# Performance work log

Hardware: AMD Instinct MI355X
Metric: run time of the kernel (lower is better)

## Reference

```python
import jax, jax.numpy as jnp
import numpy as np

B, S, D, H = 2, 2048, 1024, 16
HD = D // H  # head_dim = 64

def setup_inputs() -> dict:
    key = jax.random.key(0)
    ks = jax.random.split(key, 11)
    s = 1.0 / np.sqrt(D)
    return {
        "query_input": jax.random.normal(ks[0], (B, S, D), jnp.float32),
        "key_input":   jax.random.normal(ks[1], (B, S, D), jnp.float32),
        "value_input": jax.random.normal(ks[2], (B, S, D), jnp.float32),
        "Wq": jax.random.normal(ks[3], (D, D), jnp.float32) * s,
        "bq": jnp.zeros((D,), jnp.float32),
        "Wk": jax.random.normal(ks[4], (D, D), jnp.float32) * s,
        "bk": jnp.zeros((D,), jnp.float32),
        "Wv": jax.random.normal(ks[5], (D, D), jnp.float32) * s,
        "bv": jnp.zeros((D,), jnp.float32),
        "Wo": jax.random.normal(ks[6], (D, D), jnp.float32) * s,
        "bo": jnp.zeros((D,), jnp.float32),
    }

def _split_heads(x):
    b, s, _ = x.shape
    return x.reshape(b, s, H, HD).transpose(0, 2, 1, 3)  # [B,H,S,HD]

def reference(query_input, key_input, value_input, Wq, bq, Wk, bk, Wv, bv, Wo, bo):
    q = _split_heads(query_input @ Wq + bq)
    k = _split_heads(key_input @ Wk + bk)
    v = _split_heads(value_input @ Wv + bv)
    scores = jnp.einsum('bhqd,bhkd->bhqk', q, k) / jnp.sqrt(jnp.float32(HD))
    attn = jax.nn.softmax(scores, axis=-1)
    out = jnp.einsum('bhqk,bhkd->bhqd', attn, v)
    out = out.transpose(0, 2, 1, 3).reshape(query_input.shape[0], -1, H * HD)
    return out @ Wo + bo
```

## Files before the change

### kernel.cpp

```cpp
#include <hip/hip_runtime.h>
#include <hip/hip_bf16.h>
#include <math.h>

#define B_  2
#define S_  2048
#define D_  1024
#define H_  16
#define HD_ 64

typedef __bf16  bf16x8   __attribute__((ext_vector_type(8)));
typedef float   floatx4  __attribute__((ext_vector_type(4)));
typedef float   floatx16 __attribute__((ext_vector_type(16)));

#define MFMA16(a, b, c) __builtin_amdgcn_mfma_f32_16x16x32_bf16((a), (b), (c), 0, 0, 0)
#define MFMA32(a, b, c) __builtin_amdgcn_mfma_f32_32x32x16_bf16((a), (b), (c), 0, 0, 0)

__device__ __forceinline__ void load_lds16(const void* g, void* l) {
    __builtin_amdgcn_global_load_lds(
        (const __attribute__((address_space(1))) unsigned int*)g,
        (__attribute__((address_space(3))) unsigned int*)l, 16, 0, 0);
}

__device__ __forceinline__ unsigned pk_bf16(float a, float b) {
    unsigned r;
    asm("v_cvt_pk_bf16_f32 %0, %1, %2" : "=v"(r) : "v"(a), "v"(b));
    return r;
}

__device__ __forceinline__ float exp2_hw(float x) {
    float r;
    asm("v_exp_f32 %0, %1" : "=v"(r) : "v"(x));
    return r;
}

__global__ __launch_bounds__(256) void cast3_bf16_k(
    const float* __restrict__ x0, const float* __restrict__ x1, const float* __restrict__ x2,
    __hip_bfloat16* __restrict__ o0, __hip_bfloat16* __restrict__ o1, __hip_bfloat16* __restrict__ o2)
{
    const int z = blockIdx.y;
    const float* src = (z == 0) ? x0 : (z == 1) ? x1 : x2;
    __hip_bfloat16* dst = (z == 0) ? o0 : (z == 1) ? o1 : o2;
    const int i = blockIdx.x * 256 + threadIdx.x;
    const float4* s4 = (const float4*)src;
    const float4 a = s4[2 * i + 0];
    const float4 b = s4[2 * i + 1];
    union { __hip_bfloat16 h[8]; uint4 v; } p;
    p.h[0] = __float2bfloat16(a.x); p.h[1] = __float2bfloat16(a.y);
    p.h[2] = __float2bfloat16(a.z); p.h[3] = __float2bfloat16(a.w);
    p.h[4] = __float2bfloat16(b.x); p.h[5] = __float2bfloat16(b.y);
    p.h[6] = __float2bfloat16(b.z); p.h[7] = __float2bfloat16(b.w);
    ((uint4*)dst)[i] = p.v;
}

__global__ __launch_bounds__(256) void transpose4_cast_k(
    const float* __restrict__ W0, const float* __restrict__ W1,
    const float* __restrict__ W2, const float* __restrict__ W3,
    __hip_bfloat16* __restrict__ T0, __hip_bfloat16* __restrict__ T1,
    __hip_bfloat16* __restrict__ T2, __hip_bfloat16* __restrict__ T3)
{
    const int z = blockIdx.z;
    const float* W = (z == 0) ? W0 : (z == 1) ? W1 : (z == 2) ? W2 : W3;
    __hip_bfloat16* Wt = (z == 0) ? T0 : (z == 1) ? T1 : (z == 2) ? T2 : T3;

    __shared__ float T[64][65];
    const int t  = threadIdx.x;
    const int n0 = blockIdx.x * 64, k0 = blockIdx.y * 64;
    #pragma unroll
    for (int i = 0; i < 4; ++i) {
        const int u = t + i * 256;
        const int r = u >> 4, c4 = (u & 15) * 4;
        const float4 v = *(const float4*)(W + (size_t)(k0 + r) * D_ + n0 + c4);
        T[r][c4 + 0] = v.x; T[r][c4 + 1] = v.y; T[r][c4 + 2] = v.z; T[r][c4 + 3] = v.w;
    }
    __syncthreads();
    #pragma unroll
    for (int i = 0; i < 4; ++i) {
        const int u = t + i * 256;
        const int n = u >> 4, c4 = (u & 15) * 4;
        union { __hip_bfloat16 h[4]; uint2 v; } p;
        #pragma unroll
        for (int j = 0; j < 4; ++j) p.h[j] = __float2bfloat16(T[c4 + j][n]);
        *(uint2*)(Wt + (size_t)(n0 + n) * D_ + k0 + c4) = p.v;
    }
}

__global__ __launch_bounds__(256) void gemm_qkv_k(
    const __hip_bfloat16* __restrict__ xq, const __hip_bfloat16* __restrict__ xk,
    const __hip_bfloat16* __restrict__ xv,
    const __hip_bfloat16* __restrict__ WqT, const __hip_bfloat16* __restrict__ WkT,
    const __hip_bfloat16* __restrict__ WvT,
    const float* __restrict__ bq, const float* __restrict__ bk, const float* __restrict__ bv,
    __hip_bfloat16* __restrict__ Qh, __hip_bfloat16* __restrict__ Kh,
    __hip_bfloat16* __restrict__ Vt)
{
    constexpr int K = 1024;
    __shared__ __align__(16) short As0[128][32], As1[128][32];
    __shared__ __align__(16) short Bs0[128][32], Bs1[128][32];

    const int z = blockIdx.z;
    const __hip_bfloat16* A  = (z == 0) ? xq  : (z == 1) ? xk  : xv;
    const __hip_bfloat16* Bt = (z == 0) ? WqT : (z == 1) ? WkT : WvT;
    const float* bias        = (z == 0) ? bq  : (z == 1) ? bk  : bv;

    const int t    = threadIdx.x;
    const int lane = t & 63, w = t >> 6;
    const int quad = lane >> 4, l16 = lane & 15;
    const int m0   = blockIdx.x * 128, n0 = blockIdx.y * 128;
    const int wm   = (w >> 1) * 64,    wn = (w & 1) * 64;

    floatx4 acc[4][4] = {};

    auto stage = [&](int k0, short (*As)[32], short (*Bs)[32]) {
        #pragma unroll
        for (int i = 0; i < 2; ++i) {
            const int c = t + i * 256;
            const int m = c >> 2, kq = (c ^ (m >> 1)) & 3;
            load_lds16(A + (size_t)(m0 + m) * K + k0 + kq * 8, &As[0][0] + c * 8);
        }
        #pragma unroll
        for (int i = 0; i < 2; ++i) {
            const int c = t + i * 256;
            const int n = c >> 2, kq = (c ^ (n >> 1)) & 3;
            load_lds16(Bt + (size_t)(n0 + n) * K + k0 + kq * 8, &Bs[0][0] + c * 8);
        }
    };

    auto compute = [&](short (*As)[32], short (*Bs)[32]) {
        bf16x8 af[4], bfr[4];
        #pragma unroll
        for (int mt = 0; mt < 4; ++mt) {
            const int r = wm + mt * 16 + l16;
            af[mt]  = *(const bf16x8*)&As[r][((quad ^ (r >> 1)) & 3) * 8];
        }
        #pragma unroll
        for (int nt = 0; nt < 4; ++nt) {
            const int n = wn + nt * 16 + l16;
            bfr[nt] = *(const bf16x8*)&Bs[n][((quad ^ (n >> 1)) & 3) * 8];
        }
        #pragma unroll
        for (int mt = 0; mt < 4; ++mt)
            #pragma unroll
            for (int nt = 0; nt < 4; ++nt)
                acc[mt][nt] = MFMA16(af[mt], bfr[nt], acc[mt][nt]);
    };

    stage(0, As0, Bs0);
    for (int k0 = 0; k0 < K; k0 += 64) {
        __syncthreads();
        stage(k0 + 32, As1, Bs1);
        compute(As0, Bs0);
        __syncthreads();
        if (k0 + 64 < K) stage(k0 + 64, As0, Bs0);
        compute(As1, Bs1);
    }

    if (z != 2) {
        const float oscale = (z == 0) ? 0.125f * 1.44269504088896f : 1.0f;
        __hip_bfloat16* outp = (z == 0) ? Qh : Kh;
        #pragma unroll
        for (int mt = 0; mt < 4; ++mt)
            #pragma unroll
            for (int nt = 0; nt < 4; ++nt) {
                const int gn = n0 + wn + nt * 16 + l16;
                const float bi = bias[gn];
                #pragma unroll
                for (int r = 0; r < 4; ++r) {
                    const int gm = m0 + wm + mt * 16 + quad * 4 + r;
                    const float v = (acc[mt][nt][r] + bi) * oscale;
                    outp[(((size_t)(gm >> 11) * H_ + (gn >> 6)) * S_ + (gm & 2047)) * 64 + (gn & 63)] =
                        __float2bfloat16(v);
                }
            }
    } else {
        #pragma unroll
        for (int mt = 0; mt < 4; ++mt)
            #pragma unroll
            for (int nt = 0; nt < 4; ++nt) {
                const int gn = n0 + wn + nt * 16 + l16;
                const float bi = bias[gn];
                const int gm0 = m0 + wm + mt * 16 + quad * 4;
                union { __hip_bfloat16 h[4]; uint2 u; } pk;
                #pragma unroll
                for (int r = 0; r < 4; ++r) pk.h[r] = __float2bfloat16(acc[mt][nt][r] + bi);
                *(uint2*)(Vt + (((size_t)(gm0 >> 11) * H_ + (gn >> 6)) * 64 + (gn & 63)) * S_ +
                          (gm0 & 2047)) = pk.u;
            }
    }
}

__global__ __launch_bounds__(256) void gemm_oproj_k(
    const __hip_bfloat16* __restrict__ A, const __hip_bfloat16* __restrict__ Bt,
    const float* __restrict__ bias, float* __restrict__ out)
{
    constexpr int K = 1024, N = 1024;
    __shared__ __align__(16) short As0[128][32], As1[128][32];
    __shared__ __align__(16) short Bs0[64][32],  Bs1[64][32];

    const int t    = threadIdx.x;
    const int lane = t & 63, w = t >> 6;
    const int quad = lane >> 4, l16 = lane & 15;
    const int m0   = blockIdx.x * 128, n0 = blockIdx.y * 64;
    const int wm   = (w >> 1) * 64,    wn = (w & 1) * 32;

    floatx4 acc[4][2] = {};

    auto stage = [&](int k0, short (*As)[32], short (*Bs)[32]) {
        #pragma unroll
        for (int i = 0; i < 2; ++i) {
            const int c = t + i * 256;
            const int m = c >> 2, kq = (c ^ (m >> 1)) & 3;
            load_lds16(A + (size_t)(m0 + m) * K + k0 + kq * 8, &As[0][0] + c * 8);
        }
        {
            const int c = t;
            const int n = c >> 2, kq = (c ^ (n >> 1)) & 3;
            load_lds16(Bt + (size_t)(n0 + n) * K + k0 + kq * 8, &Bs[0][0] + c * 8);
        }
    };

    auto compute = [&](short (*As)[32], short (*Bs)[32]) {
        bf16x8 af[4], bfr[2];
        #pragma unroll
        for (int mt = 0; mt < 4; ++mt) {
            const int r = wm + mt * 16 + l16;
            af[mt]  = *(const bf16x8*)&As[r][((quad ^ (r >> 1)) & 3) * 8];
        }
        #pragma unroll
        for (int nt = 0; nt < 2; ++nt) {
            const int n = wn + nt * 16 + l16;
            bfr[nt] = *(const bf16x8*)&Bs[n][((quad ^ (n >> 1)) & 3) * 8];
        }
        #pragma unroll
        for (int mt = 0; mt < 4; ++mt)
            #pragma unroll
            for (int nt = 0; nt < 2; ++nt)
                acc[mt][nt] = MFMA16(af[mt], bfr[nt], acc[mt][nt]);
    };

    stage(0, As0, Bs0);
    for (int k0 = 0; k0 < K; k0 += 64) {
        __syncthreads();
        stage(k0 + 32, As1, Bs1);
        compute(As0, Bs0);
        __syncthreads();
        if (k0 + 64 < K) stage(k0 + 64, As0, Bs0);
        compute(As1, Bs1);
    }

    #pragma unroll
    for (int mt = 0; mt < 4; ++mt)
        #pragma unroll
        for (int nt = 0; nt < 2; ++nt) {
            const int gn = n0 + wn + nt * 16 + l16;
            const float bi = bias[gn];
            #pragma unroll
            for (int r = 0; r < 4; ++r) {
                const int gm = m0 + wm + mt * 16 + quad * 4 + r;
                out[(size_t)gm * N + gn] = acc[mt][nt][r] + bi;
            }
        }
}

union AttnSmem {
    struct { short K0[2][64][64], K1[2][64][64], V0[2][64][64], V1[2][64][64]; } s;
    struct { float O[4][64][33]; float L[4][32]; } c;
};

__global__ __launch_bounds__(512) void attn_mfma_k(
    const __hip_bfloat16* __restrict__ Qh, const __hip_bfloat16* __restrict__ Kh,
    const __hip_bfloat16* __restrict__ Vt, __hip_bfloat16* __restrict__ Ctx)
{
    __shared__ __align__(16) AttnSmem sm;

    const int t    = threadIdx.x;
    const int lane = t & 63, w = t >> 6;
    const int l32  = lane & 31, hi = lane >> 5;
    const int wq   = w & 3, half = w >> 2;
    const int ht   = t & 255;
    const int b = blockIdx.z, h = blockIdx.x;
    const size_t bh = (size_t)b * H_ + h;
    const int q0 = blockIdx.y * 128;
    const int kvbase = half * 16;

    bf16x8 qf[4];
    {
        const __hip_bfloat16* qb = Qh + (bh * S_ + q0 + wq * 32 + l32) * 64 + hi * 8;
        #pragma unroll
        for (int ks = 0; ks < 4; ++ks) qf[ks] = *(const bf16x8*)(qb + ks * 16);
    }

    floatx16 oacc[2] = {};
    float ls = 0.f;

    auto stage = [&](int kt, short (*Ks)[64], short (*Vs)[64]) {
        #pragma unroll
        for (int i = 0; i < 2; ++i) {
            const int c = ht + i * 256;
            const int p = c >> 3, kq = (c ^ p) & 7;
            load_lds16(Kh + (bh * S_ + kt * 64 + p) * 64 + kq * 8, &Ks[0][0] + c * 8);
            load_lds16(Vt + (bh * 64 + p) * S_ + kt * 64 + kq * 8, &Vs[0][0] + c * 8);
        }
    };

    auto mkfrags = [&](const float (&e)[16], bf16x8* fr) {
        #pragma unroll
        for (int k2 = 0; k2 < 2; ++k2) {
            unsigned y0 = pk_bf16(e[8 * k2 + 0], e[8 * k2 + 1]);
            unsigned y1 = pk_bf16(e[8 * k2 + 2], e[8 * k2 + 3]);
            unsigned y2 = pk_bf16(e[8 * k2 + 4], e[8 * k2 + 5]);
            unsigned y3 = pk_bf16(e[8 * k2 + 6], e[8 * k2 + 7]);
            asm volatile("v_permlane32_swap_b32 %0, %1" : "+v"(y0), "+v"(y2));
            asm volatile("v_permlane32_swap_b32 %0, %1" : "+v"(y1), "+v"(y3));
            union { unsigned u[4]; bf16x8 v; } pq;
            pq.u[0] = y0; pq.u[1] = y1; pq.u[2] = y2; pq.u[3] = y3;
            fr[k2] = pq.v;
        }
    };

    auto compute = [&](short (*Ks)[64], short (*Vs)[64]) {
        floatx16 sacc[2] = {};
        __builtin_amdgcn_s_setprio(1);
        #pragma unroll
        for (int a = 0; a < 2; ++a) {
            const int row = a * 32 + l32;
            #pragma unroll
            for (int ks = 0; ks < 4; ++ks) {
                const bf16x8 kf =
                    *(const bf16x8*)&Ks[row][(((ks * 2 + hi) ^ row) & 7) * 8];
                sacc[a] = MFMA32(kf, qf[ks], sacc[a]);
            }
        }
        __builtin_amdgcn_s_setprio(0);

        float e0[16], e1[16];
        #pragma unroll
        for (int r = 0; r < 16; ++r) { e0[r] = exp2_hw(sacc[0][r]); ls += e0[r]; }
        #pragma unroll
        for (int r = 0; r < 16; ++r) { e1[r] = exp2_hw(sacc[1][r]); ls += e1[r]; }

        bf16x8 pa[4];
        mkfrags(e0, &pa[0]);
        mkfrags(e1, &pa[2]);

        __builtin_amdgcn_s_setprio(1);
        #pragma unroll
        for (int nt = 0; nt < 2; ++nt) {
            const int row = nt * 32 + l32;
            #pragma unroll
            for (int f = 0; f < 4; ++f) {
                const bf16x8 vf =
                    *(const bf16x8*)&Vs[row][(((f * 2 + hi) ^ row) & 7) * 8];
                oacc[nt] = MFMA32(pa[f], vf, oacc[nt]);
            }
        }
        __builtin_amdgcn_s_setprio(0);
    };

    stage(kvbase, sm.s.K0[half], sm.s.V0[half]);
    for (int kt = 0; kt < 16; kt += 2) {
        __syncthreads();
        stage(kvbase + kt + 1, sm.s.K1[half], sm.s.V1[half]);
        compute(sm.s.K0[half], sm.s.V0[half]);
        __syncthreads();
        if (kt + 2 < 16) stage(kvbase + kt + 2, sm.s.K0[half], sm.s.V0[half]);
        compute(sm.s.K1[half], sm.s.V1[half]);
    }

    ls += __shfl_xor(ls, 32, 64);

    __syncthreads();
    if (half == 1) {
        #pragma unroll
        for (int nt = 0; nt < 2; ++nt)
            #pragma unroll
            for (int r = 0; r < 16; ++r)
                sm.c.O[wq][lane][nt * 16 + r] = oacc[nt][r];
        if (hi == 0) sm.c.L[wq][l32] = ls;
    }
    __syncthreads();
    if (half == 0) {
        ls += sm.c.L[wq][l32];
        const float inv = 1.0f / ls;
        float den[16];
        #pragma unroll
        for (int r = 0; r < 16; ++r)
            den[r] = __shfl(inv, (r & 3) + 8 * (r >> 2) + 4 * hi, 64);

        #pragma unroll
        for (int nt = 0; nt < 2; ++nt)
            #pragma unroll
            for (int r = 0; r < 16; ++r) {
                const int qrow = q0 + wq * 32 + (r & 3) + 8 * (r >> 2) + 4 * hi;
                const int hd   = nt * 32 + l32;
                const float o  = oacc[nt][r] + sm.c.O[wq][lane][nt * 16 + r];
                Ctx[((size_t)b * S_ + qrow) * D_ + h * 64 + hd] =
                    __float2bfloat16(o * den[r]);
            }
    }
}

extern "C" void kernel_launch(void* const* d_in, const int* in_sizes, int n_in,
                              void* d_out, int out_size, void* d_ws, size_t ws_size,
                              hipStream_t stream)
{
    const float* xq = (const float*)d_in[0];
    const float* xk = (const float*)d_in[1];
    const float* xv = (const float*)d_in[2];
    const float* Wq = (const float*)d_in[3];
    const float* bq = (const float*)d_in[4];
    const float* Wk = (const float*)d_in[5];
    const float* bk = (const float*)d_in[6];
    const float* Wv = (const float*)d_in[7];
    const float* bv = (const float*)d_in[8];
    const float* Wo = (const float*)d_in[9];
    const float* bo = (const float*)d_in[10];
    float* out = (float*)d_out;

    const size_t n = (size_t)B_ * S_ * D_;
    char* p = (char*)d_ws;
    __hip_bfloat16* xqb = (__hip_bfloat16*)p;            p += n * 2;
    __hip_bfloat16* xkb = (__hip_bfloat16*)p;            p += n * 2;
    __hip_bfloat16* xvb = (__hip_bfloat16*)p;            p += n * 2;
    __hip_bfloat16* WqT = (__hip_bfloat16*)p;            p += (size_t)D_ * D_ * 2;
    __hip_bfloat16* WkT = (__hip_bfloat16*)p;            p += (size_t)D_ * D_ * 2;
    __hip_bfloat16* WvT = (__hip_bfloat16*)p;            p += (size_t)D_ * D_ * 2;
    __hip_bfloat16* WoT = (__hip_bfloat16*)p;            p += (size_t)D_ * D_ * 2;
    __hip_bfloat16* Qh  = (__hip_bfloat16*)p;            p += n * 2;
    __hip_bfloat16* Kh  = (__hip_bfloat16*)p;            p += n * 2;
    __hip_bfloat16* Vth = (__hip_bfloat16*)p;            p += n * 2;
    __hip_bfloat16* Ctx = (__hip_bfloat16*)p;            p += n * 2;

    cast3_bf16_k<<<dim3((int)(n / 8 / 256), 3), dim3(256), 0, stream>>>(
        xq, xk, xv, xqb, xkb, xvb);
    transpose4_cast_k<<<dim3(16, 16, 4), dim3(256), 0, stream>>>(
        Wq, Wk, Wv, Wo, WqT, WkT, WvT, WoT);

    gemm_qkv_k<<<dim3((B_ * S_) / 128, D_ / 128, 3), dim3(256), 0, stream>>>(
        xqb, xkb, xvb, WqT, WkT, WvT, bq, bk, bv, Qh, Kh, Vth);

    attn_mfma_k<<<dim3(H_, S_ / 128, B_), dim3(512), 0, stream>>>(Qh, Kh, Vth, Ctx);

    gemm_oproj_k<<<dim3((B_ * S_) / 128, D_ / 64), dim3(256), 0, stream>>>(
        Ctx, WoT, bo, out);
}
```

Before: 220.3 us.

## Triple-buffer GEMM LDS staging with partial vmcnt waits and raw barriers

Both projection GEMMs move from a double buffer with two full __syncthreads per 64-wide K step to a three-buffer ring. Loads for tile k+2 are issued before computing tile k, and each step ends with a partial s_waitcnt vmcnt plus one raw s_barrier. The aim is to keep more global-to-LDS loads in flight and halve the barrier count per K step, at the cost of 50% more LDS per block. Correctness depends on the hand-coded vmcnt counts matching the number of loads issued per stage, and on the compiler not reordering LDS reads around the inline asm.

```diff
diff --git a/kernel.cpp b/kernel.cpp
--- a/kernel.cpp
+++ b/kernel.cpp
@@ -14,6 +14,9 @@
 
 #define MFMA16(a, b, c) __builtin_amdgcn_mfma_f32_16x16x32_bf16((a), (b), (c), 0, 0, 0)
 #define MFMA32(a, b, c) __builtin_amdgcn_mfma_f32_32x32x16_bf16((a), (b), (c), 0, 0, 0)
+
+#define BARRIER_RAW() asm volatile("s_barrier" ::: "memory")
+#define WAITVM(N)     asm volatile("s_waitcnt vmcnt(" #N ")" ::: "memory")
 
 __device__ __forceinline__ void load_lds16(const void* g, void* l) {
     __builtin_amdgcn_global_load_lds(
@@ -94,8 +97,8 @@
     __hip_bfloat16* __restrict__ Vt)
 {
     constexpr int K = 1024;
-    __shared__ __align__(16) short As0[128][32], As1[128][32];
-    __shared__ __align__(16) short Bs0[128][32], Bs1[128][32];
+    __shared__ __align__(16) short As0[128][32], As1[128][32], As2[128][32];
+    __shared__ __align__(16) short Bs0[128][32], Bs1[128][32], Bs2[128][32];
 
     const int z = blockIdx.z;
     const __hip_bfloat16* A  = (z == 0) ? xq  : (z == 1) ? xk  : xv;
@@ -144,14 +147,21 @@
                 acc[mt][nt] = MFMA16(af[mt], bfr[nt], acc[mt][nt]);
     };
 
-    stage(0, As0, Bs0);
-    for (int k0 = 0; k0 < K; k0 += 64) {
-        __syncthreads();
-        stage(k0 + 32, As1, Bs1);
-        compute(As0, Bs0);
-        __syncthreads();
-        if (k0 + 64 < K) stage(k0 + 64, As0, Bs0);
-        compute(As1, Bs1);
+    stage(0,  As0, Bs0);
+    stage(32, As1, Bs1);
+    WAITVM(4);
+    BARRIER_RAW();
+
+    short (*Ac)[32] = As0, (*An)[32] = As1, (*Ap)[32] = As2;
+    short (*Bc)[32] = Bs0, (*Bn)[32] = Bs1, (*Bp)[32] = Bs2;
+
+    for (int tt = 0; tt < 32; ++tt) {
+        if (tt + 2 < 32) stage((tt + 2) * 32, Ap, Bp);
+        compute(Ac, Bc);
+        if (tt < 30) WAITVM(4); else WAITVM(0);
+        BARRIER_RAW();
+        short (*ta)[32] = Ac; Ac = An; An = Ap; Ap = ta;
+        short (*tb)[32] = Bc; Bc = Bn; Bn = Bp; Bp = tb;
     }
 
     if (z != 2) {
@@ -193,8 +203,8 @@
     const float* __restrict__ bias, float* __restrict__ out)
 {
     constexpr int K = 1024, N = 1024;
-    __shared__ __align__(16) short As0[128][32], As1[128][32];
-    __shared__ __align__(16) short Bs0[64][32],  Bs1[64][32];
+    __shared__ __align__(16) short As0[128][32], As1[128][32], As2[128][32];
+    __shared__ __align__(16) short Bs0[64][32],  Bs1[64][32],  Bs2[64][32];
 
     const int t    = threadIdx.x;
     const int lane = t & 63, w = t >> 6;
@@ -237,14 +247,21 @@
                 acc[mt][nt] = MFMA16(af[mt], bfr[nt], acc[mt][nt]);
     };
 
-    stage(0, As0, Bs0);
-    for (int k0 = 0; k0 < K; k0 += 64) {
-        __syncthreads();
-        stage(k0 + 32, As1, Bs1);
-        compute(As0, Bs0);
-        __syncthreads();
-        if (k0 + 64 < K) stage(k0 + 64, As0, Bs0);
-        compute(As1, Bs1);
+    stage(0,  As0, Bs0);
+    stage(32, As1, Bs1);
+    WAITVM(3);
+    BARRIER_RAW();
+
+    short (*Ac)[32] = As0, (*An)[32] = As1, (*Ap)[32] = As2;
+    short (*Bc)[32] = Bs0, (*Bn)[32] = Bs1, (*Bp)[32] = Bs2;
+
+    for (int tt = 0; tt < 32; ++tt) {
+        if (tt + 2 < 32) stage((tt + 2) * 32, Ap, Bp);
+        compute(Ac, Bc);
+        if (tt < 30) WAITVM(3); else WAITVM(0);
+        BARRIER_RAW();
+        short (*ta)[32] = Ac; Ac = An; An = Ap; Ap = ta;
+        short (*tb)[32] = Bc; Bc = Bn; Bn = Bp; Bp = tb;
     }
 
     #pragma unroll
```

Result: no change. 222.5 us (+1.0%).

## Merge prep kernels into one launch and deepen o-proj K tile to 64

Applied to the files above, without the earlier changes.

The activation cast and weight transpose-cast kernels are combined into a single launch. Blocks in grid rows 0-2 cast the activations, and blocks in rows 3-6 transpose the weights, with any excess blocks returning early. The output-projection GEMM now stages 64-wide K tiles with an 8-chunk XOR swizzle, using one barrier per 64-K step instead of two barriers per pair of 32-K stages. The fused prep grid launches many idle blocks for the weight rows. The GEMM uses more LDS, which may lower occupancy.

```diff
diff --git a/kernel.cpp b/kernel.cpp
--- a/kernel.cpp
+++ b/kernel.cpp
@@ -33,38 +33,38 @@
     return r;
 }
 
-__global__ __launch_bounds__(256) void cast3_bf16_k(
+__global__ __launch_bounds__(256) void prep_k(
     const float* __restrict__ x0, const float* __restrict__ x1, const float* __restrict__ x2,
-    __hip_bfloat16* __restrict__ o0, __hip_bfloat16* __restrict__ o1, __hip_bfloat16* __restrict__ o2)
-{
-    const int z = blockIdx.y;
-    const float* src = (z == 0) ? x0 : (z == 1) ? x1 : x2;
-    __hip_bfloat16* dst = (z == 0) ? o0 : (z == 1) ? o1 : o2;
-    const int i = blockIdx.x * 256 + threadIdx.x;
-    const float4* s4 = (const float4*)src;
-    const float4 a = s4[2 * i + 0];
-    const float4 b = s4[2 * i + 1];
-    union { __hip_bfloat16 h[8]; uint4 v; } p;
-    p.h[0] = __float2bfloat16(a.x); p.h[1] = __float2bfloat16(a.y);
-    p.h[2] = __float2bfloat16(a.z); p.h[3] = __float2bfloat16(a.w);
-    p.h[4] = __float2bfloat16(b.x); p.h[5] = __float2bfloat16(b.y);
-    p.h[6] = __float2bfloat16(b.z); p.h[7] = __float2bfloat16(b.w);
-    ((uint4*)dst)[i] = p.v;
-}
-
-__global__ __launch_bounds__(256) void transpose4_cast_k(
+    __hip_bfloat16* __restrict__ o0, __hip_bfloat16* __restrict__ o1, __hip_bfloat16* __restrict__ o2,
     const float* __restrict__ W0, const float* __restrict__ W1,
     const float* __restrict__ W2, const float* __restrict__ W3,
     __hip_bfloat16* __restrict__ T0, __hip_bfloat16* __restrict__ T1,
     __hip_bfloat16* __restrict__ T2, __hip_bfloat16* __restrict__ T3)
 {
-    const int z = blockIdx.z;
+    const int y = blockIdx.y;
+    const int t = threadIdx.x;
+    if (y < 3) {
+        const float* src = (y == 0) ? x0 : (y == 1) ? x1 : x2;
+        __hip_bfloat16* dst = (y == 0) ? o0 : (y == 1) ? o1 : o2;
+        const int i = blockIdx.x * 256 + t;
+        const float4* s4 = (const float4*)src;
+        const float4 a = s4[2 * i + 0];
+        const float4 b = s4[2 * i + 1];
+        union { __hip_bfloat16 h[8]; uint4 v; } p;
+        p.h[0] = __float2bfloat16(a.x); p.h[1] = __float2bfloat16(a.y);
+        p.h[2] = __float2bfloat16(a.z); p.h[3] = __float2bfloat16(a.w);
+        p.h[4] = __float2bfloat16(b.x); p.h[5] = __float2bfloat16(b.y);
+        p.h[6] = __float2bfloat16(b.z); p.h[7] = __float2bfloat16(b.w);
+        ((uint4*)dst)[i] = p.v;
+        return;
+    }
+    if (blockIdx.x >= 256) return;
+    const int z = y - 3;
     const float* W = (z == 0) ? W0 : (z == 1) ? W1 : (z == 2) ? W2 : W3;
     __hip_bfloat16* Wt = (z == 0) ? T0 : (z == 1) ? T1 : (z == 2) ? T2 : T3;
 
     __shared__ float T[64][65];
-    const int t  = threadIdx.x;
-    const int n0 = blockIdx.x * 64, k0 = blockIdx.y * 64;
+    const int n0 = (blockIdx.x & 15) * 64, k0 = (blockIdx.x >> 4) * 64;
     #pragma unroll
     for (int i = 0; i < 4; ++i) {
         const int u = t + i * 256;
@@ -193,8 +193,8 @@
     const float* __restrict__ bias, float* __restrict__ out)
 {
     constexpr int K = 1024, N = 1024;
-    __shared__ __align__(16) short As0[128][32], As1[128][32];
-    __shared__ __align__(16) short Bs0[64][32],  Bs1[64][32];
+    __shared__ __align__(16) short As[2][128][64];
+    __shared__ __align__(16) short Bs[2][64][64];
 
     const int t    = threadIdx.x;
     const int lane = t & 63, w = t >> 6;
@@ -204,47 +204,49 @@
 
     floatx4 acc[4][2] = {};
 
-    auto stage = [&](int k0, short (*As)[32], short (*Bs)[32]) {
+    auto stage = [&](int k0, int buf) {
+        #pragma unroll
+        for (int i = 0; i < 4; ++i) {
+            const int c = t + i * 256;
+            const int m = c >> 3, kq = (c ^ m) & 7;
+            load_lds16(A + (size_t)(m0 + m) * K + k0 + kq * 8, &As[buf][0][0] + c * 8);
+        }
         #pragma unroll
         for (int i = 0; i < 2; ++i) {
             const int c = t + i * 256;
-            const int m = c >> 2, kq = (c ^ (m >> 1)) & 3;
-            load_lds16(A + (size_t)(m0 + m) * K + k0 + kq * 8, &As[0][0] + c * 8);
-        }
-        {
-            const int c = t;
-            const int n = c >> 2, kq = (c ^ (n >> 1)) & 3;
-            load_lds16(Bt + (size_t)(n0 + n) * K + k0 + kq * 8, &Bs[0][0] + c * 8);
-        }
-    };
-
-    auto compute = [&](short (*As)[32], short (*Bs)[32]) {
-        bf16x8 af[4], bfr[2];
-        #pragma unroll
-        for (int mt = 0; mt < 4; ++mt) {
-            const int r = wm + mt * 16 + l16;
-            af[mt]  = *(const bf16x8*)&As[r][((quad ^ (r >> 1)) & 3) * 8];
-        }
-        #pragma unroll
-        for (int nt = 0; nt < 2; ++nt) {
-            const int n = wn + nt * 16 + l16;
-            bfr[nt] = *(const bf16x8*)&Bs[n][((quad ^ (n >> 1)) & 3) * 8];
-        }
-        #pragma unroll
-        for (int mt = 0; mt < 4; ++mt)
-            #pragma unroll
-            for (int nt = 0; nt < 2; ++nt)
-                acc[mt][nt] = MFMA16(af[mt], bfr[nt], acc[mt][nt]);
-    };
-
-    stage(0, As0, Bs0);
-    for (int k0 = 0; k0 < K; k0 += 64) {
+            const int n = c >> 3, kq = (c ^ n) & 7;
+            load_lds16(Bt + (size_t)(n0 + n) * K + k0 + kq * 8, &Bs[buf][0][0] + c * 8);
+        }
+    };
+
+    auto compute64 = [&](int buf) {
+        #pragma unroll
+        for (int ks = 0; ks < 2; ++ks) {
+            bf16x8 af[4], bfr[2];
+            const int ch = ks * 4 + quad;
+            #pragma unroll
+            for (int mt = 0; mt < 4; ++mt) {
+                const int r = wm + mt * 16 + l16;
+                af[mt]  = *(const bf16x8*)&As[buf][r][((ch ^ r) & 7) * 8];
+            }
+            #pragma unroll
+            for (int nt = 0; nt < 2; ++nt) {
+                const int n = wn + nt * 16 + l16;
+                bfr[nt] = *(const bf16x8*)&Bs[buf][n][((ch ^ n) & 7) * 8];
+            }
+            #pragma unroll
+            for (int mt = 0; mt < 4; ++mt)
+                #pragma unroll
+                for (int nt = 0; nt < 2; ++nt)
+                    acc[mt][nt] = MFMA16(af[mt], bfr[nt], acc[mt][nt]);
+        }
+    };
+
+    stage(0, 0);
+    for (int tt = 0; tt < 16; ++tt) {
         __syncthreads();
-        stage(k0 + 32, As1, Bs1);
-        compute(As0, Bs0);
-        __syncthreads();
-        if (k0 + 64 < K) stage(k0 + 64, As0, Bs0);
-        compute(As1, Bs1);
+        if (tt + 1 < 16) stage((tt + 1) * 64, (tt + 1) & 1);
+        compute64(tt & 1);
     }
 
     #pragma unroll
@@ -430,10 +432,8 @@
     __hip_bfloat16* Vth = (__hip_bfloat16*)p;            p += n * 2;
     __hip_bfloat16* Ctx = (__hip_bfloat16*)p;            p += n * 2;
 
-    cast3_bf16_k<<<dim3((int)(n / 8 / 256), 3), dim3(256), 0, stream>>>(
-        xq, xk, xv, xqb, xkb, xvb);
-    transpose4_cast_k<<<dim3(16, 16, 4), dim3(256), 0, stream>>>(
-        Wq, Wk, Wv, Wo, WqT, WkT, WvT, WoT);
+    prep_k<<<dim3((int)(n / 8 / 256), 7), dim3(256), 0, stream>>>(
+        xq, xk, xv, xqb, xkb, xvb, Wq, Wk, Wv, Wo, WqT, WkT, WvT, WoT);
 
     gemm_qkv_k<<<dim3((B_ * S_) / 128, D_ / 128, 3), dim3(256), 0, stream>>>(
         xqb, xkb, xvb, WqT, WkT, WvT, bq, bk, bv, Qh, Kh, Vth);
```

Result: no change. 221.5 us (+0.5%).
